# Performance work log

Hardware: AMD Instinct MI355X
Metric: run time of the kernel (lower is better)

## Reference

```python
import jax, jax.numpy as jnp
import numpy as np
import math

N_NODES = 64000
N_GRAPHS = 512
HIDDEN = 128
CLUSTERS = 10
NUM_FILTER = 16
N_CLASSES = 2
S_HID = math.ceil((HIDDEN + CLUSTERS) / 2)  # 69
P_HID = 8


def _mlp2(x, w1, b1, w2, b2):
    # 2-layer MLP: Linear -> ReLU -> Linear (matches MLP(2, in, hid, out))
    return jax.nn.relu(x @ w1 + b1) @ w2 + b2


def setup_inputs() -> dict:
    key = jax.random.key(0)
    ks = jax.random.split(key, 12)
    # node embeddings (output of get_emb)
    H_all = jax.random.normal(ks[0], (N_NODES, HIDDEN), dtype=jnp.float32)
    # graph indicator: 125 nodes per graph, sorted (as produced by batching)
    batch = jnp.repeat(jnp.arange(N_GRAPHS, dtype=jnp.int32), N_NODES // N_GRAPHS)
    targets = jax.random.randint(ks[1], (N_GRAPHS,), 0, N_CLASSES, dtype=jnp.int32)
    s = 0.05
    # S_mlp: hidden -> S_HID -> clusters
    w1 = jax.random.normal(ks[2], (HIDDEN, S_HID), dtype=jnp.float32) * s
    b1 = jnp.zeros((S_HID,), dtype=jnp.float32)
    w2 = jax.random.normal(ks[3], (S_HID, CLUSTERS), dtype=jnp.float32) * s
    b2 = jnp.zeros((CLUSTERS,), dtype=jnp.float32)
    # final: hidden*clusters -> 2
    wf = jax.random.normal(ks[4], (HIDDEN * CLUSTERS, N_CLASSES), dtype=jnp.float32) * s
    bf = jnp.zeros((N_CLASSES,), dtype=jnp.float32)
    # prototype_features_MLP: hidden -> 8 -> num_graph_filter
    p1 = jax.random.normal(ks[5], (HIDDEN, P_HID), dtype=jnp.float32) * s
    pb1 = jnp.zeros((P_HID,), dtype=jnp.float32)
    p2 = jax.random.normal(ks[6], (P_HID, NUM_FILTER), dtype=jnp.float32) * s
    pb2 = jnp.zeros((NUM_FILTER,), dtype=jnp.float32)
    # correlation parameters (initialized like the torch module)
    corr_inter = jax.nn.softmax(jax.random.uniform(ks[7], (N_CLASSES, NUM_FILTER)), axis=0)
    corr_intra = jax.nn.softmax(jax.random.uniform(ks[8], (N_CLASSES, NUM_FILTER)), axis=1)
    return {"H_all": H_all, "batch": batch, "targets": targets,
            "w1": w1, "b1": b1, "w2": w2, "b2": b2,
            "wf": wf, "bf": bf,
            "p1": p1, "pb1": pb1, "p2": p2, "pb2": pb2,
            "corr_inter": corr_inter, "corr_intra": corr_intra}


def reference(H_all, batch, targets, w1, b1, w2, b2, wf, bf,
              p1, pb1, p2, pb2, corr_inter, corr_intra):
    # per-node soft cluster assignment  [N, C]
    S_all = jax.nn.softmax(_mlp2(H_all, w1, b1, w2, b2), axis=-1)
    # segment matmul E_g = S_g^T @ H_g  -> [B, C, D] via segment-reduced outer products
    outer = S_all[:, :, None] * H_all[:, None, :]  # [N, C, D]
    E_all = jax.ops.segment_sum(outer, batch, num_segments=N_GRAPHS)
    B = E_all.shape[0]
    pred1 = E_all.reshape(B, -1) @ wf + bf  # dropout off (eval)
    p = jax.nn.softmax(pred1, axis=-1)
    # multinomial sample from pred_softmax (no grad)
    key = jax.random.key(42)
    sample = jax.random.categorical(key, jnp.log(jax.lax.stop_gradient(p) + 1e-12), axis=-1)
    ind_positive_sample = sample == targets
    oh = jax.nn.one_hot(sample, N_CLASSES, dtype=p.dtype)
    epsilon = jax.lax.stop_gradient(jnp.where(oh != 0, 1.0 - p, -p))
    sample_cat_oh = p + epsilon  # straight-through one-hot
    Q = jax.nn.softmax(_mlp2(E_all, p1, pb1, p2, pb2), axis=-1)  # [B, C, F]
    correlation = jax.nn.softmax(corr_inter, axis=0) * jax.nn.softmax(corr_intra, axis=1)  # [2, F]
    correlation_mask = sample_cat_oh @ correlation  # [B, F]
    feature_mask = jnp.sum(Q * correlation_mask[:, None, :], axis=-1)  # [B, C]
    E_masked = feature_mask[:, :, None] * E_all  # einsum('bi,bij->bij')
    pred2 = E_masked.reshape(B, -1) @ wf + bf
    return (pred1, pred2, ind_positive_sample, S_all, E_all, Q)
```

## Files before the change

kernel.cpp:

```cpp
#include <hip/hip_runtime.h>

#define NN 64000
#define NG 512
#define NPG 125
#define DIM 128
#define NC 10
#define SHID 69
#define NF 16
#define PHID 8
#define ELPAD 132
#define TSTR 85
#define PSTR 41

#define OFF_PRED1 0
#define OFF_PRED2 1024
#define OFF_IND   2048
#define OFF_S     2560
#define OFF_E     642560
#define OFF_Q     1297920

typedef __attribute__((ext_vector_type(8))) short short8;
typedef __attribute__((ext_vector_type(4))) float f32x4;

__device__ __forceinline__ unsigned rotl32(unsigned x, int r) {
    return (x << r) | (x >> (32 - r));
}

__device__ __forceinline__ void threefry_0_42(unsigned x0, unsigned x1,
                                              unsigned& o0, unsigned& o1) {
    const unsigned k0 = 0u, k1 = 42u;
    const unsigned k2 = k0 ^ k1 ^ 0x1BD11BDAu;
    unsigned ks[3] = {k0, k1, k2};
    const int R0[4] = {13, 15, 26, 6};
    const int R1[4] = {17, 29, 16, 24};
    x0 += k0; x1 += k1;
    #pragma unroll
    for (int i = 0; i < 5; i++) {
        const int* R = (i & 1) ? R1 : R0;
        #pragma unroll
        for (int r = 0; r < 4; r++) {
            x0 += x1;
            x1 = rotl32(x1, R[r]);
            x1 ^= x0;
        }
        x0 += ks[(i + 1) % 3];
        x1 += ks[(i + 2) % 3] + (unsigned)(i + 1);
    }
    o0 = x0; o1 = x1;
}

__device__ __forceinline__ unsigned random_bits_partitionable(unsigned i) {
    unsigned o0, o1;
    threefry_0_42(0u, i, o0, o1);
    return o0 ^ o1;
}

__device__ __forceinline__ float gumbel_from_bits(unsigned bits) {
    float f = __uint_as_float((bits >> 9) | 0x3f800000u) - 1.0f;
    if (f <= 0.0f) f = 1.1754943508222875e-38f;
    return -logf(-logf(f));
}

#define R10(M) M(0) M(1) M(2) M(3) M(4) M(5) M(6) M(7) M(8) M(9)

__global__ __launch_bounds__(256, 4) void k_node_mlp(
    const float* __restrict__ H, const float* __restrict__ w1,
    const float* __restrict__ b1, const float* __restrict__ w2,
    const float* __restrict__ b2, float* __restrict__ S) {
    __shared__ __align__(16) char lds[40960];
    short* fragHi = (short*)lds;
    short* fragLo = (short*)(lds + 20480);
    int tid = threadIdx.x;

    for (int s = tid; s < 1280; s += 256) {
        int jt = s >> 8, ks = (s >> 6) & 3, l = s & 63;
        int j = jt * 16 + (l & 15);
        int kb = ks * 32 + ((l >> 4) & 3) * 8;
        short8 vh, vl;
        #pragma unroll
        for (int i = 0; i < 8; i++) {
            float x = (j < SHID) ? w1[(kb + i) * SHID + j] : 0.0f;
            unsigned u = __float_as_uint(x);
            vh[i] = (short)(u >> 16);
            float hf = __uint_as_float(u & 0xFFFF0000u);
            float lo = x - hf;
            vl[i] = (short)(__float_as_uint(lo) >> 16);
        }
        *(short8*)(fragHi + (size_t)s * 8) = vh;
        *(short8*)(fragLo + (size_t)s * 8) = vl;
    }
    __syncthreads();

    int w = tid >> 6, l = tid & 63;
    int node = blockIdx.x * 64 + w * 16 + (l & 15);
    const float* Hp = H + (size_t)node * DIM + ((l >> 4) & 3) * 8;

    short8 aHi[4], aLo[4];
    #pragma unroll
    for (int ks = 0; ks < 4; ks++) {
        float4 x0 = *(const float4*)(Hp + ks * 32);
        float4 x1 = *(const float4*)(Hp + ks * 32 + 4);
        float xs[8] = {x0.x, x0.y, x0.z, x0.w, x1.x, x1.y, x1.z, x1.w};
        #pragma unroll
        for (int i = 0; i < 8; i++) {
            unsigned u = __float_as_uint(xs[i]);
            aHi[ks][i] = (short)(u >> 16);
            float lo = xs[i] - __uint_as_float(u & 0xFFFF0000u);
            aLo[ks][i] = (short)(__float_as_uint(lo) >> 16);
        }
    }

    f32x4 acc[5];
    #pragma unroll
    for (int jt = 0; jt < 5; jt++) {
        f32x4 a = {0.f, 0.f, 0.f, 0.f};
        #pragma unroll
        for (int ks = 0; ks < 4; ks++) {
            int slot = (jt * 4 + ks) * 64 + l;
            short8 bh = *(short8*)(fragHi + (size_t)slot * 8);
            short8 bl = *(short8*)(fragLo + (size_t)slot * 8);
            a = __builtin_amdgcn_mfma_f32_16x16x32_bf16(aHi[ks], bh, a, 0, 0, 0);
            a = __builtin_amdgcn_mfma_f32_16x16x32_bf16(aLo[ks], bh, a, 0, 0, 0);
            a = __builtin_amdgcn_mfma_f32_16x16x32_bf16(aHi[ks], bl, a, 0, 0, 0);
        }
        acc[jt] = a;
    }
    __syncthreads();

    float* Ts = (float*)lds;
    float* Ps = (float*)(lds + 21760);
    #pragma unroll
    for (int jt = 0; jt < 5; jt++) {
        int j = jt * 16 + (l & 15);
        float bj = (j < SHID) ? b1[j] : 0.0f;
        #pragma unroll
        for (int r = 0; r < 4; r++) {
            int m = w * 16 + ((l >> 4) & 3) * 4 + r;
            float tv = acc[jt][r];
            Ts[m * TSTR + j] = (j < SHID) ? fmaxf(tv + bj, 0.0f) : 0.0f;
        }
    }
    __syncthreads();

    {
        int n = tid & 63, q = tid >> 6;
        float lg[NC] = {};
        for (int jj = 0; jj < 18; jj++) {
            int j = q * 18 + jj;
            int jx = (j < SHID) ? j : (SHID - 1);
            float tr = Ts[n * TSTR + j];
            const float* w2r = w2 + jx * NC;
            #pragma unroll
            for (int c = 0; c < NC; c++) lg[c] = fmaf(tr, w2r[c], lg[c]);
        }
        #pragma unroll
        for (int c = 0; c < NC; c++) Ps[n * PSTR + q * NC + c] = lg[c];
    }
    __syncthreads();

    if (tid < 64) {
        int n = tid;
        const float* pr = &Ps[n * PSTR];
        #define LD(c) float s##c = pr[c] + pr[10 + c] + pr[20 + c] + pr[30 + c] + b2[c];
        R10(LD)
        #undef LD
        float m = fmaxf(fmaxf(fmaxf(s0, s1), fmaxf(s2, s3)),
                        fmaxf(fmaxf(fmaxf(s4, s5), fmaxf(s6, s7)), fmaxf(s8, s9)));
        float e0 = expf(s0 - m), e1 = expf(s1 - m), e2 = expf(s2 - m),
              e3 = expf(s3 - m), e4 = expf(s4 - m), e5 = expf(s5 - m),
              e6 = expf(s6 - m), e7 = expf(s7 - m), e8 = expf(s8 - m),
              e9 = expf(s9 - m);
        float ssum = ((e0 + e1) + (e2 + e3)) + ((e4 + e5) + (e6 + e7)) + (e8 + e9);
        float inv = 1.0f / ssum;
        float2* Sp2 = (float2*)(S + ((size_t)blockIdx.x * 64 + n) * NC);
        Sp2[0] = make_float2(e0 * inv, e1 * inv);
        Sp2[1] = make_float2(e2 * inv, e3 * inv);
        Sp2[2] = make_float2(e4 * inv, e5 * inv);
        Sp2[3] = make_float2(e6 * inv, e7 * inv);
        Sp2[4] = make_float2(e8 * inv, e9 * inv);
    }
}

__global__ __launch_bounds__(512, 2) void k_E_tail(
    const float* __restrict__ H, const float* __restrict__ S,
    const float* __restrict__ wf, const float* __restrict__ bf,
    const int* __restrict__ targets,
    const float* __restrict__ p1, const float* __restrict__ pb1,
    const float* __restrict__ p2, const float* __restrict__ pb2,
    const float* __restrict__ ci, const float* __restrict__ cr,
    float* __restrict__ E, float* __restrict__ pred1, float* __restrict__ pred2,
    float* __restrict__ ind, float* __restrict__ Q) {
    __shared__ __align__(8) float Sl[128 * NC];
    __shared__ float Epart[3 * 128 * NC];
    __shared__ __align__(16) float El[NC * ELPAD];
    __shared__ float fmbuf[NC];
    int g = blockIdx.x, tid = threadIdx.x;

    const float* Sg = S + (size_t)g * NPG * NC;
    for (int i = tid; i < 128 * NC; i += 512) Sl[i] = (i < NPG * NC) ? Sg[i] : 0.0f;
    __syncthreads();

    int q = tid >> 7;
    int d = tid & 127;
    const float* Hg = H + (size_t)g * NPG * DIM + d;

    #define DECLA(c) float a##c = 0.f;
    R10(DECLA)
    #undef DECLA
    int n0 = q * 32;
    #pragma unroll
    for (int ib = 0; ib < 32; ib += 4) {
        float h[4];
        #pragma unroll
        for (int u = 0; u < 4; u++) {
            int nh = min(n0 + ib + u, NPG - 1);
            h[u] = Hg[(size_t)nh * DIM];
        }
        #pragma unroll
        for (int u = 0; u < 4; u++) {
            const float2* S2 = (const float2*)(Sl + (n0 + ib + u) * NC);
            float2 s01 = S2[0], s23 = S2[1], s45 = S2[2], s67 = S2[3], s89 = S2[4];
            a0 = fmaf(s01.x, h[u], a0); a1 = fmaf(s01.y, h[u], a1);
            a2 = fmaf(s23.x, h[u], a2); a3 = fmaf(s23.y, h[u], a3);
            a4 = fmaf(s45.x, h[u], a4); a5 = fmaf(s45.y, h[u], a5);
            a6 = fmaf(s67.x, h[u], a6); a7 = fmaf(s67.y, h[u], a7);
            a8 = fmaf(s89.x, h[u], a8); a9 = fmaf(s89.y, h[u], a9);
        }
    }
    if (q > 0) {
        float* ep = &Epart[(q - 1) * 128 * NC + d * NC];
        #define STP(c) ep[c] = a##c;
        R10(STP)
        #undef STP
    }
    __syncthreads();
    if (q == 0) {
        const float* e1p = &Epart[d * NC];
        const float* e2p = &Epart[128 * NC + d * NC];
        const float* e3p = &Epart[2 * 128 * NC + d * NC];
        float* Eo = E + (size_t)g * (NC * DIM) + d;
        #define CMB(c) { a##c += e1p[c] + e2p[c] + e3p[c]; \
                         El[c * ELPAD + d] = a##c; Eo[c * DIM] = a##c; }
        R10(CMB)
        #undef CMB
    }
    __syncthreads();

    const float2* wf2 = (const float2*)wf;
    int l = tid;
    int samp = 0;
    float corr_lf = 0.f;

    if (tid < 64) {
        if (l < 32) {
            int i = l >> 4, f = l & 15;
            float a = ci[f], b = ci[NF + f];
            float mm = fmaxf(a, b);
            float ea = expf(a - mm), eb = expf(b - mm);
            float inter = expf(ci[i * NF + f] - mm) / (ea + eb);
            float mi = -1e30f;
            for (int j = 0; j < NF; j++) mi = fmaxf(mi, cr[i * NF + j]);
            float ri = 0.f;
            for (int j = 0; j < NF; j++) ri += expf(cr[i * NF + j] - mi);
            float intra = expf(cr[i * NF + f] - mi) / ri;
            corr_lf = inter * intra;
        }

        float a0 = 0.f, a1 = 0.f;
        #pragma unroll
        for (int i = 0; i < 20; i++) {
            int idx = i * 64 + l;
            float e = El[(idx >> 7) * ELPAD + (idx & 127)];
            float2 w = wf2[idx];
            a0 = fmaf(e, w.x, a0);
            a1 = fmaf(e, w.y, a1);
        }
        #pragma unroll
        for (int off = 32; off > 0; off >>= 1) {
            a0 += __shfl_down(a0, off);
            a1 += __shfl_down(a1, off);
        }
        if (l == 0) {
            float y0 = a0 + bf[0], y1 = a1 + bf[1];
            pred1[g * 2] = y0;
            pred1[g * 2 + 1] = y1;
            float m = fmaxf(y0, y1);
            float e0 = expf(y0 - m), e1 = expf(y1 - m), s = e0 + e1;
            float p0 = e0 / s, pp1 = e1 / s;
            float g0 = gumbel_from_bits(random_bits_partitionable(2 * g));
            float g1 = gumbel_from_bits(random_bits_partitionable(2 * g + 1));
            float l0 = logf(p0 + 1e-12f) + g0;
            float l1 = logf(pp1 + 1e-12f) + g1;
            samp = (l1 > l0) ? 1 : 0;
            ind[g] = (samp == targets[g]) ? 1.0f : 0.0f;
        }
        samp = __shfl(samp, 0);

        if (l < 40) {
            int p = l >> 2, s = l & 3;
            float ua = pb1[2 * s], ub = pb1[2 * s + 1];
            const float4* E4 = (const float4*)&El[p * ELPAD];
            #pragma unroll 4
            for (int k4 = 0; k4 < 32; k4++) {
                float4 e4 = E4[k4];
                float es[4] = {e4.x, e4.y, e4.z, e4.w};
                #pragma unroll
                for (int kk = 0; kk < 4; kk++) {
                    int k = k4 * 4 + kk;
                    ua = fmaf(es[kk], p1[k * PHID + 2 * s], ua);
                    ub = fmaf(es[kk], p1[k * PHID + 2 * s + 1], ub);
                }
            }
            ua = fmaxf(ua, 0.f);
            ub = fmaxf(ub, 0.f);
            float v[NF];
            #pragma unroll
            for (int f = 0; f < NF; f++) {
                v[f] = pb2[f] * 0.25f;
                v[f] = fmaf(ua, p2[(2 * s) * NF + f], v[f]);
                v[f] = fmaf(ub, p2[(2 * s + 1) * NF + f], v[f]);
            }
            #pragma unroll
            for (int f = 0; f < NF; f++) {
                v[f] += __shfl_xor(v[f], 1);
                v[f] += __shfl_xor(v[f], 2);
            }
            float m = v[0];
            #pragma unroll
            for (int f = 1; f < NF; f++) m = fmaxf(m, v[f]);
            float ssum = 0.f, qv[NF];
            #pragma unroll
            for (int f = 0; f < NF; f++) { qv[f] = expf(v[f] - m); ssum += qv[f]; }
            float inv = 1.0f / ssum;
            #pragma unroll
            for (int f = 0; f < NF; f++) qv[f] *= inv;
            float* Qo = Q + ((size_t)g * NC + p) * NF;
            ((float4*)Qo)[s] = make_float4(qv[s * 4], qv[s * 4 + 1], qv[s * 4 + 2], qv[s * 4 + 3]);
            float fmv = 0.f;
            #pragma unroll
            for (int f = 0; f < NF; f++) {
                float cv = __shfl(corr_lf, samp * NF + f);
                fmv = fmaf(qv[f], cv, fmv);
            }
            if (s == 0) fmbuf[p] = fmv;
        }
    }
    __syncthreads();

    if (tid < 64) {
        float b0 = 0.f, b1acc = 0.f;
        #pragma unroll
        for (int i = 0; i < 20; i++) {
            int idx = i * 64 + l;
            float e = El[(idx >> 7) * ELPAD + (idx & 127)] * fmbuf[idx >> 7];
            float2 w = wf2[idx];
            b0 = fmaf(e, w.x, b0);
            b1acc = fmaf(e, w.y, b1acc);
        }
        #pragma unroll
        for (int off = 32; off > 0; off >>= 1) {
            b0 += __shfl_down(b0, off);
            b1acc += __shfl_down(b1acc, off);
        }
        if (l == 0) {
            pred2[g * 2] = b0 + bf[0];
            pred2[g * 2 + 1] = b1acc + bf[1];
        }
    }
}

extern "C" void kernel_launch(void* const* d_in, const int* in_sizes, int n_in,
                              void* d_out, int out_size, void* d_ws, size_t ws_size,
                              hipStream_t stream) {
    const float* H       = (const float*)d_in[0];
    const int*   targets = (const int*)d_in[2];
    const float* w1      = (const float*)d_in[3];
    const float* b1      = (const float*)d_in[4];
    const float* w2      = (const float*)d_in[5];
    const float* b2      = (const float*)d_in[6];
    const float* wf      = (const float*)d_in[7];
    const float* bf      = (const float*)d_in[8];
    const float* p1      = (const float*)d_in[9];
    const float* pb1     = (const float*)d_in[10];
    const float* p2      = (const float*)d_in[11];
    const float* pb2     = (const float*)d_in[12];
    const float* ci      = (const float*)d_in[13];
    const float* cr      = (const float*)d_in[14];

    float* out   = (float*)d_out;
    float* pred1 = out + OFF_PRED1;
    float* pred2 = out + OFF_PRED2;
    float* ind   = out + OFF_IND;
    float* S     = out + OFF_S;
    float* E     = out + OFF_E;
    float* Q     = out + OFF_Q;

    k_node_mlp<<<NN / 64, 256, 0, stream>>>(H, w1, b1, w2, b2, S);
    k_E_tail<<<NG, 512, 0, stream>>>(H, S, wf, bf, targets, p1, pb1, p2, pb2,
                                     ci, cr, E, pred1, pred2, ind, Q);
}
```

Before: 127.0 us.

## Precompute w1 bf16 split once and widen segment-sum blocks to 1024 threads

Moves the per-block bf16 hi/lo splitting of w1 out of the node MLP kernel into a small separate kernel that writes MFMA-ready fragments to workspace. The node MLP blocks then read the B fragments straight from global memory, which drops the per-block prologue and barrier and frees LDS for occupancy. The segment-sum tail kernel now uses 1024 threads (8 node slices of 16 rows instead of 4 of 32), with a padded partial-sum buffer and a 7-way reduction. The cost is an extra kernel launch, fragment reads from global/L2 instead of LDS, and a larger reduction with a heavier block.

```diff
diff --git a/kernel.cpp b/kernel.cpp
--- a/kernel.cpp
+++ b/kernel.cpp
@@ -11,6 +11,7 @@
 #define ELPAD 132
 #define TSTR 85
 #define PSTR 41
+#define EPSTR 11
 
 #define OFF_PRED1 0
 #define OFF_PRED2 1024
@@ -63,34 +64,31 @@
 
 #define R10(M) M(0) M(1) M(2) M(3) M(4) M(5) M(6) M(7) M(8) M(9)
 
+__global__ __launch_bounds__(256) void k_split_w1(
+    const float* __restrict__ w1, short* __restrict__ fragHi,
+    short* __restrict__ fragLo) {
+    int e = blockIdx.x * 256 + threadIdx.x;
+    int s = e >> 3, i = e & 7;
+    int jt = s >> 8, ks = (s >> 6) & 3, l = s & 63;
+    int j = jt * 16 + (l & 15);
+    int kb = ks * 32 + ((l >> 4) & 3) * 8;
+    float x = (j < SHID) ? w1[(kb + i) * SHID + j] : 0.0f;
+    unsigned u = __float_as_uint(x);
+    short hi = (short)(u >> 16);
+    float hf = __uint_as_float(u & 0xFFFF0000u);
+    short lo = (short)(__float_as_uint(x - hf) >> 16);
+    fragHi[s * 8 + i] = hi;
+    fragLo[s * 8 + i] = lo;
+}
+
 __global__ __launch_bounds__(256, 4) void k_node_mlp(
-    const float* __restrict__ H, const float* __restrict__ w1,
+    const float* __restrict__ H, const short* __restrict__ fragHi,
+    const short* __restrict__ fragLo,
     const float* __restrict__ b1, const float* __restrict__ w2,
     const float* __restrict__ b2, float* __restrict__ S) {
-    __shared__ __align__(16) char lds[40960];
-    short* fragHi = (short*)lds;
-    short* fragLo = (short*)(lds + 20480);
+    __shared__ __align__(16) float Ts[64 * TSTR];
+    __shared__ float Ps[64 * PSTR];
     int tid = threadIdx.x;
-
-    for (int s = tid; s < 1280; s += 256) {
-        int jt = s >> 8, ks = (s >> 6) & 3, l = s & 63;
-        int j = jt * 16 + (l & 15);
-        int kb = ks * 32 + ((l >> 4) & 3) * 8;
-        short8 vh, vl;
-        #pragma unroll
-        for (int i = 0; i < 8; i++) {
-            float x = (j < SHID) ? w1[(kb + i) * SHID + j] : 0.0f;
-            unsigned u = __float_as_uint(x);
-            vh[i] = (short)(u >> 16);
-            float hf = __uint_as_float(u & 0xFFFF0000u);
-            float lo = x - hf;
-            vl[i] = (short)(__float_as_uint(lo) >> 16);
-        }
-        *(short8*)(fragHi + (size_t)s * 8) = vh;
-        *(short8*)(fragLo + (size_t)s * 8) = vl;
-    }
-    __syncthreads();
-
     int w = tid >> 6, l = tid & 63;
     int node = blockIdx.x * 64 + w * 16 + (l & 15);
     const float* Hp = H + (size_t)node * DIM + ((l >> 4) & 3) * 8;
@@ -117,18 +115,15 @@
         #pragma unroll
         for (int ks = 0; ks < 4; ks++) {
             int slot = (jt * 4 + ks) * 64 + l;
-            short8 bh = *(short8*)(fragHi + (size_t)slot * 8);
-            short8 bl = *(short8*)(fragLo + (size_t)slot * 8);
+            short8 bh = *(const short8*)(fragHi + (size_t)slot * 8);
+            short8 bl = *(const short8*)(fragLo + (size_t)slot * 8);
             a = __builtin_amdgcn_mfma_f32_16x16x32_bf16(aHi[ks], bh, a, 0, 0, 0);
             a = __builtin_amdgcn_mfma_f32_16x16x32_bf16(aLo[ks], bh, a, 0, 0, 0);
             a = __builtin_amdgcn_mfma_f32_16x16x32_bf16(aHi[ks], bl, a, 0, 0, 0);
         }
         acc[jt] = a;
     }
-    __syncthreads();
-
-    float* Ts = (float*)lds;
-    float* Ps = (float*)(lds + 21760);
+
     #pragma unroll
     for (int jt = 0; jt < 5; jt++) {
         int j = jt * 16 + (l & 15);
@@ -181,7 +176,7 @@
     }
 }
 
-__global__ __launch_bounds__(512, 2) void k_E_tail(
+__global__ __launch_bounds__(1024, 4) void k_E_tail(
     const float* __restrict__ H, const float* __restrict__ S,
     const float* __restrict__ wf, const float* __restrict__ bf,
     const int* __restrict__ targets,
@@ -191,13 +186,13 @@
     float* __restrict__ E, float* __restrict__ pred1, float* __restrict__ pred2,
     float* __restrict__ ind, float* __restrict__ Q) {
     __shared__ __align__(8) float Sl[128 * NC];
-    __shared__ float Epart[3 * 128 * NC];
+    __shared__ float Epart[7 * 128 * EPSTR];
     __shared__ __align__(16) float El[NC * ELPAD];
     __shared__ float fmbuf[NC];
     int g = blockIdx.x, tid = threadIdx.x;
 
     const float* Sg = S + (size_t)g * NPG * NC;
-    for (int i = tid; i < 128 * NC; i += 512) Sl[i] = (i < NPG * NC) ? Sg[i] : 0.0f;
+    for (int i = tid; i < 128 * NC; i += 1024) Sl[i] = (i < NPG * NC) ? Sg[i] : 0.0f;
     __syncthreads();
 
     int q = tid >> 7;
@@ -207,17 +202,17 @@
     #define DECLA(c) float a##c = 0.f;
     R10(DECLA)
     #undef DECLA
-    int n0 = q * 32;
+    int n0 = q * 16;
     #pragma unroll
-    for (int ib = 0; ib < 32; ib += 4) {
-        float h[4];
-        #pragma unroll
-        for (int u = 0; u < 4; u++) {
+    for (int ib = 0; ib < 16; ib += 8) {
+        float h[8];
+        #pragma unroll
+        for (int u = 0; u < 8; u++) {
             int nh = min(n0 + ib + u, NPG - 1);
             h[u] = Hg[(size_t)nh * DIM];
         }
         #pragma unroll
-        for (int u = 0; u < 4; u++) {
+        for (int u = 0; u < 8; u++) {
             const float2* S2 = (const float2*)(Sl + (n0 + ib + u) * NC);
             float2 s01 = S2[0], s23 = S2[1], s45 = S2[2], s67 = S2[3], s89 = S2[4];
             a0 = fmaf(s01.x, h[u], a0); a1 = fmaf(s01.y, h[u], a1);
@@ -228,19 +223,21 @@
         }
     }
     if (q > 0) {
-        float* ep = &Epart[(q - 1) * 128 * NC + d * NC];
+        float* ep = &Epart[((q - 1) * 128 + d) * EPSTR];
         #define STP(c) ep[c] = a##c;
         R10(STP)
         #undef STP
     }
     __syncthreads();
     if (q == 0) {
-        const float* e1p = &Epart[d * NC];
-        const float* e2p = &Epart[128 * NC + d * NC];
-        const float* e3p = &Epart[2 * 128 * NC + d * NC];
         float* Eo = E + (size_t)g * (NC * DIM) + d;
-        #define CMB(c) { a##c += e1p[c] + e2p[c] + e3p[c]; \
-                         El[c * ELPAD + d] = a##c; Eo[c * DIM] = a##c; }
+        #pragma unroll
+        for (int k = 0; k < 7; k++) {
+            const float* ep = &Epart[(k * 128 + d) * EPSTR];
+            a0 += ep[0]; a1 += ep[1]; a2 += ep[2]; a3 += ep[3]; a4 += ep[4];
+            a5 += ep[5]; a6 += ep[6]; a7 += ep[7]; a8 += ep[8]; a9 += ep[9];
+        }
+        #define CMB(c) { El[(c) * ELPAD + d] = a##c; Eo[(c) * DIM] = a##c; }
         R10(CMB)
         #undef CMB
     }
@@ -395,7 +392,11 @@
     float* E     = out + OFF_E;
     float* Q     = out + OFF_Q;
 
-    k_node_mlp<<<NN / 64, 256, 0, stream>>>(H, w1, b1, w2, b2, S);
-    k_E_tail<<<NG, 512, 0, stream>>>(H, S, wf, bf, targets, p1, pb1, p2, pb2,
-                                     ci, cr, E, pred1, pred2, ind, Q);
-}
+    short* fragHi = (short*)d_ws;
+    short* fragLo = (short*)((char*)d_ws + 20480);
+
+    k_split_w1<<<40, 256, 0, stream>>>(w1, fragHi, fragLo);
+    k_node_mlp<<<NN / 64, 256, 0, stream>>>(H, fragHi, fragLo, b1, w2, b2, S);
+    k_E_tail<<<NG, 1024, 0, stream>>>(H, S, wf, bf, targets, p1, pb1, p2, pb2,
+                                      ci, cr, E, pred1, pred2, ind, Q);
+}
```

Result: slower. 132.6 us (+4.4%).
